# Kernel tuning notes

Measured on AMD Instinct MI355X. Metric: run time of the kernel, lower is better.

Reference implementation:

```python
import jax, jax.numpy as jnp
import numpy as np

DIM = 768
HEADS = 12
HEAD_DIM = DIM // HEADS
SCALE = HEAD_DIM ** -0.5


def setup_inputs() -> dict:
    key = jax.random.key(0)
    k1, k2, k3, k4 = jax.random.split(key, 4)
    x = jax.random.normal(k1, (8, 1025, DIM), dtype=jnp.float32)
    # torch nn.Linear weight layout: (out_features, in_features)
    w_qkv = jax.random.normal(k2, (3 * DIM, DIM), dtype=jnp.float32) * (DIM ** -0.5)
    w_proj = jax.random.normal(k3, (DIM, DIM), dtype=jnp.float32) * (DIM ** -0.5)
    b_proj = jax.random.normal(k4, (DIM,), dtype=jnp.float32) * 0.01
    return {"x": x, "w_qkv": w_qkv, "w_proj": w_proj, "b_proj": b_proj}


def reference(x, w_qkv, w_proj, b_proj):
    B, N, C = x.shape
    H, D = HEADS, HEAD_DIM
    # qkv: (B, N, 3C) -> (3, B, H, N, D)
    qkv = jnp.einsum('bnc,oc->bno', x, w_qkv)
    qkv = qkv.reshape(B, N, 3, H, D).transpose(2, 0, 3, 1, 4)
    q, k, v = qkv[0], qkv[1], qkv[2]
    attn = jnp.einsum('bhnd,bhmd->bhnm', q, k) * SCALE
    attn = jax.nn.softmax(attn, axis=-1)
    out = jnp.einsum('bhnm,bhmd->bhnd', attn, v)
    out = out.transpose(0, 2, 1, 3).reshape(B, N, C)
    out = jnp.einsum('bnc,oc->bno', out, w_proj) + b_proj
    return out
```

## Files before the change

### kernel.cpp

```cpp
#include <hip/hip_runtime.h>
#include <stdint.h>

#define DIMC 768
#define NSEQ 1025
#define BATCH 8
#define HEADS 12
#define HDIM 64
#define OC3 2304
#define MROWS (BATCH * NSEQ)
#define NBH (BATCH * HEADS)
#define KVB 64
#define NT 17
#define QTILE 128
#define NQT 9
#define VSTRIDE (NT * KVB)
#define C2 0.1803368801111244f
#define OFFB (-11.541560327111707f)

typedef short bf16x8 __attribute__((ext_vector_type(8)));
typedef float f32x4 __attribute__((ext_vector_type(4)));
typedef float f32x16 __attribute__((ext_vector_type(16)));
typedef uint32_t u32x4 __attribute__((ext_vector_type(4)));

__device__ __forceinline__ uint32_t f2bf(float x) {
    uint32_t u = __builtin_bit_cast(uint32_t, x);
    return (u + 0x7fffu + ((u >> 16) & 1u)) >> 16;
}
__device__ __forceinline__ float4 ld4(const float* p) {
    return *reinterpret_cast<const float4*>(p);
}
__device__ __forceinline__ uint32_t cvtpk(float lo, float hi) {
    uint32_t r;
    asm("v_cvt_pk_bf16_f32 %0, %1, %2" : "=v"(r) : "v"(lo), "v"(hi));
    return r;
}
__device__ __forceinline__ void plswap(uint32_t& x, uint32_t& y) {
    asm volatile("v_permlane32_swap_b32 %0, %1" : "+v"(x), "+v"(y));
}
__device__ __forceinline__ void async_cp16(void* lds, const void* g) {
    __builtin_amdgcn_global_load_lds(
        (const __attribute__((address_space(1))) uint32_t*)g,
        (__attribute__((address_space(3))) uint32_t*)lds, 16, 0, 0);
}

__global__ __launch_bounds__(256) void cvt_all(const float* __restrict__ x,
                                               const float* __restrict__ wq,
                                               const float* __restrict__ wp,
                                               uint16_t* __restrict__ xb,
                                               uint16_t* __restrict__ wqb,
                                               uint16_t* __restrict__ wpb) {
    const int NX = MROWS * DIMC / 8, NQ = OC3 * DIMC / 8, NP = DIMC * DIMC / 8;
    const int i = blockIdx.x * 256 + threadIdx.x;
    const float* src;
    uint16_t* dst;
    int off;
    if (i < NX)                { src = x;  dst = xb;  off = i; }
    else if (i < NX + NQ)      { src = wq; dst = wqb; off = i - NX; }
    else if (i < NX + NQ + NP) { src = wp; dst = wpb; off = i - NX - NQ; }
    else return;
    const float4 a = ld4(src + off * 8), b = ld4(src + off * 8 + 4);
    uint4 o;
    o.x = f2bf(a.x) | (f2bf(a.y) << 16);
    o.y = f2bf(a.z) | (f2bf(a.w) << 16);
    o.z = f2bf(b.x) | (f2bf(b.y) << 16);
    o.w = f2bf(b.z) | (f2bf(b.w) << 16);
    *reinterpret_cast<uint4*>(dst + off * 8) = o;
}

template <bool OUTBF, bool BIAS>
__global__ __launch_bounds__(256) void gemm_bf16_nt(const uint16_t* __restrict__ A,
                                                    const uint16_t* __restrict__ W,
                                                    const float* __restrict__ bias,
                                                    void* __restrict__ Out,
                                                    int M, int N, int K) {
    __shared__ __align__(16) char smem[32768];
    char* const As = smem;
    char* const Ws = smem + 16384;

    const int tid = threadIdx.x;
    const int wave = tid >> 6, lane = tid & 63;
    const int l15 = lane & 15, l4 = lane >> 4;
    const int wr = wave >> 1, wc = wave & 1;
    const int m0 = blockIdx.y * 128, n0 = blockIdx.x * 128;

    f32x4 acc[4][4] = {};

    int srow[4], scol[4];
#pragma unroll
    for (int i = 0; i < 4; ++i) {
        const int X = i * 4096 + wave * 1024 + lane * 16;
        const int row = X >> 7;
        const int slot = (X & 127) >> 4;
        srow[i] = row;
        scol[i] = (slot ^ (row & 7)) << 3;
    }

    for (int kt = 0; kt < K; kt += 64) {
        __syncthreads();
#pragma unroll
        for (int i = 0; i < 4; ++i) {
            int am = m0 + srow[i];
            if (am >= M) am = M - 1;
            async_cp16(As + i * 4096 + wave * 1024,
                       A + (size_t)am * K + kt + scol[i]);
            const int wn = n0 + srow[i];
            async_cp16(Ws + i * 4096 + wave * 1024,
                       W + (size_t)wn * K + kt + scol[i]);
        }
        __syncthreads();

#pragma unroll
        for (int ch = 0; ch < 2; ++ch) {
            const int kb = (ch << 6) + (l4 << 4);
            bf16x8 af[4], bw[4];
#pragma unroll
            for (int mi = 0; mi < 4; ++mi) {
                const int row = wr * 64 + mi * 16 + l15;
                af[mi] = *(const bf16x8*)(As + (row << 7) + (kb ^ ((row & 7) << 4)));
            }
#pragma unroll
            for (int nj = 0; nj < 4; ++nj) {
                const int row = wc * 64 + nj * 16 + l15;
                bw[nj] = *(const bf16x8*)(Ws + (row << 7) + (kb ^ ((row & 7) << 4)));
            }
#pragma unroll
            for (int mi = 0; mi < 4; ++mi)
#pragma unroll
                for (int nj = 0; nj < 4; ++nj)
                    acc[mi][nj] = __builtin_amdgcn_mfma_f32_16x16x32_bf16(
                        af[mi], bw[nj], acc[mi][nj], 0, 0, 0);
        }
    }

#pragma unroll
    for (int mi = 0; mi < 4; ++mi) {
#pragma unroll
        for (int r = 0; r < 4; ++r) {
            const int m = m0 + wr * 64 + mi * 16 + l4 * 4 + r;
            if (m < M) {
#pragma unroll
                for (int nj = 0; nj < 4; ++nj) {
                    const int n = n0 + wc * 64 + nj * 16 + l15;
                    float v = acc[mi][nj][r];
                    if (BIAS) v += bias[n];
                    if (OUTBF)
                        ((uint16_t*)Out)[(size_t)m * N + n] = (uint16_t)f2bf(v);
                    else
                        ((float*)Out)[(size_t)m * N + n] = v;
                }
            }
        }
    }
}

__global__ __launch_bounds__(256) void transpose_v(const uint16_t* __restrict__ qkv,
                                                   uint16_t* __restrict__ vt) {
    const int kt = blockIdx.x, bh = blockIdx.y;
    const int h = bh % HEADS, b = bh / HEADS;
    __shared__ __align__(16) char lds[8192];
    const int tid = threadIdx.x;
    const uint16_t* src = qkv + (size_t)b * NSEQ * OC3 + 2 * DIMC + h * HDIM;
    uint16_t* dst = vt + (size_t)bh * HDIM * VSTRIDE + kt * KVB;

#pragma unroll
    for (int i = 0; i < 2; ++i) {
        const int s = i * 256 + tid;
        const int kv = s >> 3, c = s & 7;
        int kvg = kt * KVB + kv;
        if (kvg > NSEQ - 1) kvg = NSEQ - 1;
        const uint4 d4 = *(const uint4*)(src + (size_t)kvg * OC3 + c * 8);
        *(uint4*)(lds + (kv << 7) + ((c ^ (kv & 7)) << 4)) = d4;
    }
    __syncthreads();

#pragma unroll
    for (int i = 0; i < 2; ++i) {
        const int s = i * 256 + tid;
        const int d = s >> 3, c = s & 7;
        uint32_t w[4];
#pragma unroll
        for (int p = 0; p < 4; ++p) {
            const int k0 = c * 8 + p * 2, k1 = k0 + 1;
            const uint32_t lo = *(const uint16_t*)(lds + (k0 << 7) +
                ((((d >> 3) ^ (k0 & 7)) << 4) + ((d & 7) << 1)));
            const uint32_t hi = *(const uint16_t*)(lds + (k1 << 7) +
                ((((d >> 3) ^ (k1 & 7)) << 4) + ((d & 7) << 1)));
            w[p] = lo | (hi << 16);
        }
        uint4 o4;
        o4.x = w[0]; o4.y = w[1]; o4.z = w[2]; o4.w = w[3];
        *(uint4*)(dst + (size_t)d * VSTRIDE + c * 8) = o4;
    }
}

__global__ __launch_bounds__(256) void flash_attn2(const uint16_t* __restrict__ qkv,
                                                   const uint16_t* __restrict__ vt,
                                                   uint16_t* __restrict__ out) {
    const int wg = blockIdx.x;
    const int lg = (wg & 7) * 108 + (wg >> 3);
    const int qt = lg % NQT;
    const int bh = lg / NQT;
    const int h = bh % HEADS, b = bh / HEADS;

    const int tid = threadIdx.x;
    const int wave = tid >> 6, lane = tid & 63;
    const int l31 = lane & 31, lh = lane >> 5;

    __shared__ __align__(16) char smem[32768];

    const uint16_t* Kg = qkv + (size_t)b * NSEQ * OC3 + DIMC + h * HDIM;
    const uint16_t* Vt = vt + (size_t)bh * HDIM * VSTRIDE;

    bf16x8 qf[4];
    {
        int qrow = qt * QTILE + wave * 32 + l31;
        if (qrow > NSEQ - 1) qrow = NSEQ - 1;
        const uint16_t* Qg = qkv + (size_t)(b * NSEQ + qrow) * OC3 + h * HDIM;
#pragma unroll
        for (int ds = 0; ds < 4; ++ds)
            qf[ds] = *(const bf16x8*)(Qg + ds * 16 + lh * 8);
    }

    bf16x8 ones;
#pragma unroll
    for (int i = 0; i < 8; ++i) ones[i] = (short)0x3F80;

    auto stageK = [&](int kv0, char* Kb) {
#pragma unroll
        for (int i = 0; i < 2; ++i) {
            const int X = i * 4096 + wave * 1024 + lane * 16;
            const int row = X >> 7;
            const int slot = (X & 127) >> 4;
            int kvg = kv0 + row;
            if (kvg > NSEQ - 1) kvg = NSEQ - 1;
            async_cp16(Kb + i * 4096 + wave * 1024,
                       Kg + (size_t)kvg * OC3 + ((slot ^ (row & 7)) << 3));
        }
    };
    auto stageV = [&](int kv0, char* Vb) {
#pragma unroll
        for (int i = 0; i < 2; ++i) {
            const int X = i * 4096 + wave * 1024 + lane * 16;
            const int d = X >> 7;
            const int slot = (X & 127) >> 4;
            async_cp16(Vb + i * 4096 + wave * 1024,
                       Vt + (size_t)d * VSTRIDE + kv0 + ((slot ^ (d & 7)) << 3));
        }
    };

    stageK(0, smem);
    stageV(0, smem + 16384);
    __syncthreads();

    f32x16 o[2] = {};
    f32x16 osum = {};

    for (int t = 0; t < NT; ++t) {
        const int cur = t & 1;
        const int kv0 = t * KVB;
        char* const Kc = smem + cur * 8192;
        char* const Vc = smem + 16384 + cur * 8192;

        if (t < NT - 1) {
            stageK(kv0 + KVB, smem + (cur ^ 1) * 8192);
            stageV(kv0 + KVB, smem + 16384 + (cur ^ 1) * 8192);
        }

        f32x16 s[2] = {};
        __builtin_amdgcn_s_setprio(1);
#pragma unroll
        for (int kvb = 0; kvb < 2; ++kvb) {
            const int krow = kvb * 32 + l31;
            const int kbase = (krow << 7);
            const int sw = (l31 & 7) << 4;
#pragma unroll
            for (int ds = 0; ds < 4; ++ds) {
                bf16x8 kf = *(const bf16x8*)(Kc + kbase + ((ds * 32 + lh * 16) ^ sw));
                s[kvb] = __builtin_amdgcn_mfma_f32_32x32x16_bf16(kf, qf[ds], s[kvb], 0, 0, 0);
            }
        }
        __builtin_amdgcn_s_setprio(0);

        if (t == NT - 1) {
#pragma unroll
            for (int kvb = 0; kvb < 2; ++kvb)
#pragma unroll
                for (int r = 0; r < 16; ++r) {
                    const int kvg = kv0 + kvb * 32 + (r & 3) + 8 * (r >> 2) + 4 * lh;
                    if (kvg >= NSEQ) s[kvb][r] = -INFINITY;
                }
        }

#pragma unroll
        for (int kvb = 0; kvb < 2; ++kvb)
#pragma unroll
            for (int r = 0; r < 16; ++r)
                s[kvb][r] = __builtin_amdgcn_exp2f(fmaf(s[kvb][r], C2, OFFB));

        bf16x8 pa[4];
#pragma unroll
        for (int kb = 0; kb < 4; ++kb) {
            const f32x16 S = s[kb >> 1];
            const int c = (kb & 1) * 8;
            uint32_t w0 = cvtpk(S[c + 0], S[c + 1]);
            uint32_t w2 = cvtpk(S[c + 4], S[c + 5]);
            plswap(w0, w2);
            uint32_t w1 = cvtpk(S[c + 2], S[c + 3]);
            uint32_t w3 = cvtpk(S[c + 6], S[c + 7]);
            plswap(w1, w3);
            u32x4 w;
            w[0] = w0; w[1] = w1; w[2] = w2; w[3] = w3;
            pa[kb] = __builtin_bit_cast(bf16x8, w);
        }

        __builtin_amdgcn_s_setprio(1);
#pragma unroll
        for (int kb = 0; kb < 4; ++kb)
            osum = __builtin_amdgcn_mfma_f32_32x32x16_bf16(ones, pa[kb], osum, 0, 0, 0);
#pragma unroll
        for (int db = 0; db < 2; ++db) {
            const int d = db * 32 + l31;
            const int dbase = (d << 7);
            const int sw = (l31 & 7) << 4;
#pragma unroll
            for (int kb = 0; kb < 4; ++kb) {
                bf16x8 vf = *(const bf16x8*)(Vc + dbase + ((kb * 32 + lh * 16) ^ sw));
                o[db] = __builtin_amdgcn_mfma_f32_32x32x16_bf16(vf, pa[kb], o[db], 0, 0, 0);
            }
        }
        __builtin_amdgcn_s_setprio(0);

        if (t < NT - 1) __syncthreads();
    }

    {
        const int qrow = qt * QTILE + wave * 32 + l31;
        if (qrow < NSEQ) {
            const float inv = 1.0f / osum[0];
            uint16_t* orow = out + (size_t)(b * NSEQ + qrow) * DIMC + h * HDIM;
#pragma unroll
            for (int db = 0; db < 2; ++db)
#pragma unroll
                for (int g = 0; g < 4; ++g) {
                    const int d = db * 32 + g * 8 + lh * 4;
                    uint2 ww;
                    ww.x = cvtpk(o[db][g * 4 + 0] * inv, o[db][g * 4 + 1] * inv);
                    ww.y = cvtpk(o[db][g * 4 + 2] * inv, o[db][g * 4 + 3] * inv);
                    *(uint2*)(orow + d) = ww;
                }
        }
    }
}

extern "C" void kernel_launch(void* const* d_in, const int* in_sizes, int n_in,
                              void* d_out, int out_size, void* d_ws, size_t ws_size,
                              hipStream_t stream) {
    const float* x      = (const float*)d_in[0];
    const float* w_qkv  = (const float*)d_in[1];
    const float* w_proj = (const float*)d_in[2];
    const float* b_proj = (const float*)d_in[3];
    float* out = (float*)d_out;

    const size_t NVT = (size_t)NBH * HDIM * VSTRIDE;
    uint16_t* xb   = (uint16_t*)d_ws;
    uint16_t* wqb  = xb  + (size_t)MROWS * DIMC;
    uint16_t* wpb  = wqb + (size_t)OC3 * DIMC;
    uint16_t* qkv  = wpb + (size_t)DIMC * DIMC;
    uint16_t* vt   = qkv + (size_t)MROWS * OC3;
    uint16_t* attb = vt + NVT;

    const dim3 blk(256);
    const int ncvt = (MROWS * DIMC + OC3 * DIMC + DIMC * DIMC) / 8;
    cvt_all<<<dim3((ncvt + 255) / 256), blk, 0, stream>>>(x, w_qkv, w_proj, xb, wqb, wpb);

    gemm_bf16_nt<true, false><<<dim3(OC3 / 128, (MROWS + 127) / 128), blk, 0, stream>>>(
        xb, wqb, nullptr, qkv, MROWS, OC3, DIMC);

    transpose_v<<<dim3(NT, NBH), blk, 0, stream>>>(qkv, vt);

    flash_attn2<<<dim3(NQT * HEADS * BATCH), blk, 0, stream>>>(qkv, vt, attb);

    gemm_bf16_nt<false, true><<<dim3(DIMC / 128, (MROWS + 127) / 128), blk, 0, stream>>>(
        attb, wpb, b_proj, out, MROWS, DIMC, DIMC);
}
```

Measured before the change: 131.6 us.

## Split attention KV loop into two halves and merge partials in a combine kernel

Each (batch, head, query tile) attention block is now split into two workgroups. One covers KV tiles 0-8 and the other covers tiles 9-16, which doubles the grid and is meant to improve CU load balance and reduce the tail. Each half writes an unnormalized bf16 partial output and its float row-sum. A new combine kernel adds the two partials, divides by the total row-sum and writes the attention output. The split relies on the softmax using a fixed offset rather than a running max, so the partials can simply be added. In exchange it adds an extra launch, extra global traffic for the partials, and bf16 rounding of the unnormalized partial outputs.

```diff
diff --git a/kernel.cpp b/kernel.cpp
--- a/kernel.cpp
+++ b/kernel.cpp
@@ -13,6 +13,7 @@
 #define NT 17
 #define QTILE 128
 #define NQT 9
+#define HTILES 9
 #define VSTRIDE (NT * KVB)
 #define C2 0.1803368801111244f
 #define OFFB (-11.541560327111707f)
@@ -25,6 +26,9 @@
 __device__ __forceinline__ uint32_t f2bf(float x) {
     uint32_t u = __builtin_bit_cast(uint32_t, x);
     return (u + 0x7fffu + ((u >> 16) & 1u)) >> 16;
+}
+__device__ __forceinline__ float bf2f(uint32_t b) {
+    return __builtin_bit_cast(float, b << 16);
 }
 __device__ __forceinline__ float4 ld4(const float* p) {
     return *reinterpret_cast<const float4*>(p);
@@ -153,8 +157,8 @@
     }
 }
 
-__global__ __launch_bounds__(256) void transpose_v(const uint16_t* __restrict__ qkv,
-                                                   uint16_t* __restrict__ vt) {
+__global__ __launch_bounds__(256) void vtrans(const uint16_t* __restrict__ qkv,
+                                              uint16_t* __restrict__ vt) {
     const int kt = blockIdx.x, bh = blockIdx.y;
     const int h = bh % HEADS, b = bh / HEADS;
     __shared__ __align__(16) char lds[8192];
@@ -195,11 +199,14 @@
 
 __global__ __launch_bounds__(256) void flash_attn2(const uint16_t* __restrict__ qkv,
                                                    const uint16_t* __restrict__ vt,
-                                                   uint16_t* __restrict__ out) {
+                                                   uint16_t* __restrict__ opart,
+                                                   float* __restrict__ lpart) {
     const int wg = blockIdx.x;
-    const int lg = (wg & 7) * 108 + (wg >> 3);
+    const int lg = (wg & 7) * 216 + (wg >> 3);
     const int qt = lg % NQT;
-    const int bh = lg / NQT;
+    const int g = lg / NQT;
+    const int bh = g >> 1;
+    const int half = g & 1;
     const int h = bh % HEADS, b = bh / HEADS;
 
     const int tid = threadIdx.x;
@@ -248,20 +255,23 @@
         }
     };
 
-    stageK(0, smem);
-    stageV(0, smem + 16384);
+    const int tstart = half * HTILES;
+    const int tend = half ? NT : HTILES;
+
+    stageK(tstart * KVB, smem);
+    stageV(tstart * KVB, smem + 16384);
     __syncthreads();
 
     f32x16 o[2] = {};
     f32x16 osum = {};
 
-    for (int t = 0; t < NT; ++t) {
-        const int cur = t & 1;
+    for (int t = tstart; t < tend; ++t) {
+        const int cur = (t - tstart) & 1;
         const int kv0 = t * KVB;
         char* const Kc = smem + cur * 8192;
         char* const Vc = smem + 16384 + cur * 8192;
 
-        if (t < NT - 1) {
+        if (t < tend - 1) {
             stageK(kv0 + KVB, smem + (cur ^ 1) * 8192);
             stageV(kv0 + KVB, smem + 16384 + (cur ^ 1) * 8192);
         }
@@ -330,26 +340,60 @@
         }
         __builtin_amdgcn_s_setprio(0);
 
-        if (t < NT - 1) __syncthreads();
+        if (t < tend - 1) __syncthreads();
     }
 
     {
         const int qrow = qt * QTILE + wave * 32 + l31;
         if (qrow < NSEQ) {
-            const float inv = 1.0f / osum[0];
-            uint16_t* orow = out + (size_t)(b * NSEQ + qrow) * DIMC + h * HDIM;
+            const size_t row = ((size_t)half * NBH + bh) * NSEQ + qrow;
+            uint16_t* orow = opart + row * HDIM;
 #pragma unroll
             for (int db = 0; db < 2; ++db)
 #pragma unroll
-                for (int g = 0; g < 4; ++g) {
-                    const int d = db * 32 + g * 8 + lh * 4;
+                for (int g4 = 0; g4 < 4; ++g4) {
+                    const int d = db * 32 + g4 * 8 + lh * 4;
                     uint2 ww;
-                    ww.x = cvtpk(o[db][g * 4 + 0] * inv, o[db][g * 4 + 1] * inv);
-                    ww.y = cvtpk(o[db][g * 4 + 2] * inv, o[db][g * 4 + 3] * inv);
+                    ww.x = cvtpk(o[db][g4 * 4 + 0], o[db][g4 * 4 + 1]);
+                    ww.y = cvtpk(o[db][g4 * 4 + 2], o[db][g4 * 4 + 3]);
                     *(uint2*)(orow + d) = ww;
                 }
-        }
-    }
+            if (lh == 0) lpart[row] = osum[0];
+        }
+    }
+}
+
+__global__ __launch_bounds__(256) void combine(const uint16_t* __restrict__ opart,
+                                               const float* __restrict__ lpart,
+                                               uint16_t* __restrict__ attb) {
+    const int gid = blockIdx.x * 256 + threadIdx.x;
+    if (gid >= NBH * NSEQ * 8) return;
+    const int oct = gid & 7;
+    const int t = gid >> 3;
+    const int bh = t / NSEQ;
+    const int q = t - bh * NSEQ;
+    const int h = bh % HEADS, b = bh / HEADS;
+    const size_t HALF = (size_t)NBH * NSEQ;
+
+    const uint4 o1 = *(const uint4*)(opart + (size_t)t * HDIM + oct * 8);
+    const uint4 o2 = *(const uint4*)(opart + (HALF + t) * HDIM + oct * 8);
+    const float inv = 1.0f / (lpart[t] + lpart[HALF + t]);
+
+    const uint32_t a[4] = {o1.x, o1.y, o1.z, o1.w};
+    const uint32_t c[4] = {o2.x, o2.y, o2.z, o2.w};
+    uint2 w0, w1;
+    float v[8];
+#pragma unroll
+    for (int p = 0; p < 4; ++p) {
+        v[p * 2 + 0] = (bf2f(a[p] & 0xffffu) + bf2f(c[p] & 0xffffu)) * inv;
+        v[p * 2 + 1] = (bf2f(a[p] >> 16) + bf2f(c[p] >> 16)) * inv;
+    }
+    w0.x = cvtpk(v[0], v[1]); w0.y = cvtpk(v[2], v[3]);
+    w1.x = cvtpk(v[4], v[5]); w1.y = cvtpk(v[6], v[7]);
+
+    uint16_t* dst = attb + ((size_t)b * NSEQ + q) * DIMC + h * HDIM + oct * 8;
+    *(uint2*)dst = w0;
+    *(uint2*)(dst + 4) = w1;
 }
 
 extern "C" void kernel_launch(void* const* d_in, const int* in_sizes, int n_in,
@@ -362,12 +406,15 @@
     float* out = (float*)d_out;
 
     const size_t NVT = (size_t)NBH * HDIM * VSTRIDE;
-    uint16_t* xb   = (uint16_t*)d_ws;
-    uint16_t* wqb  = xb  + (size_t)MROWS * DIMC;
-    uint16_t* wpb  = wqb + (size_t)OC3 * DIMC;
-    uint16_t* qkv  = wpb + (size_t)DIMC * DIMC;
-    uint16_t* vt   = qkv + (size_t)MROWS * OC3;
-    uint16_t* attb = vt + NVT;
+    const size_t NOP = (size_t)2 * NBH * NSEQ * HDIM;
+    uint16_t* xb    = (uint16_t*)d_ws;
+    uint16_t* wqb   = xb  + (size_t)MROWS * DIMC;
+    uint16_t* wpb   = wqb + (size_t)OC3 * DIMC;
+    uint16_t* qkv   = wpb + (size_t)DIMC * DIMC;
+    uint16_t* vt    = qkv + (size_t)MROWS * OC3;
+    uint16_t* opart = vt + NVT;
+    float*    lpart = (float*)(opart + NOP);
+    uint16_t* attb  = (uint16_t*)(lpart + (size_t)2 * NBH * NSEQ);
 
     const dim3 blk(256);
     const int ncvt = (MROWS * DIMC + OC3 * DIMC + DIMC * DIMC) / 8;
@@ -376,9 +423,11 @@
     gemm_bf16_nt<true, false><<<dim3(OC3 / 128, (MROWS + 127) / 128), blk, 0, stream>>>(
         xb, wqb, nullptr, qkv, MROWS, OC3, DIMC);
 
-    transpose_v<<<dim3(NT, NBH), blk, 0, stream>>>(qkv, vt);
-
-    flash_attn2<<<dim3(NQT * HEADS * BATCH), blk, 0, stream>>>(qkv, vt, attb);
+    vtrans<<<dim3(NT, NBH), blk, 0, stream>>>(qkv, vt);
+
+    flash_attn2<<<dim3(NQT * NBH * 2), blk, 0, stream>>>(qkv, vt, opart, lpart);
+
+    combine<<<dim3((NBH * NSEQ * 8 + 255) / 256), blk, 0, stream>>>(opart, lpart, attb);
 
     gemm_bf16_nt<false, true><<<dim3(DIMC / 128, (MROWS + 127) / 128), blk, 0, stream>>>(
         attb, wpb, b_proj, out, MROWS, DIMC, DIMC);
```

After: 136.1 us. 3.4% more time.
